# Performance work log

Measured on AMD Instinct MI355X. Metric: run time of the kernel, lower is better.

## Reference

```python
import jax, jax.numpy as jnp
import numpy as np

EMBED_DIM = 768
Q_DIM = 64
V_DIM = 64
WINDOW_SIZE = 3


def setup_inputs() -> dict:
    key = jax.random.key(0)
    ks = jax.random.split(key, 7)
    B, N = 4, 4096
    s = 1.0 / np.sqrt(EMBED_DIM)
    x = jax.random.normal(ks[0], (B, N, EMBED_DIM), dtype=jnp.float32)
    Wq = jax.random.normal(ks[1], (EMBED_DIM, Q_DIM), dtype=jnp.float32) * s
    bq = jax.random.normal(ks[2], (Q_DIM,), dtype=jnp.float32) * 0.01
    Wk = jax.random.normal(ks[3], (EMBED_DIM, Q_DIM), dtype=jnp.float32) * s
    bk = jax.random.normal(ks[4], (Q_DIM,), dtype=jnp.float32) * 0.01
    Wv = jax.random.normal(ks[5], (EMBED_DIM, V_DIM), dtype=jnp.float32) * s
    bv = jax.random.normal(ks[6], (V_DIM,), dtype=jnp.float32) * 0.01
    return {"x": x, "Wq": Wq, "bq": bq, "Wk": Wk, "bk": bk, "Wv": Wv, "bv": bv}


def reference(x, Wq, bq, Wk, bk, Wv, bv):
    # Faithful translation of SliddingWindowAttention.forward, including the
    # original's quirk: diagonal scores are written into columns 0..window_size-1
    # of a full (B, N, N) zero matrix, softmax is taken over ALL N columns
    # (zeros included), and the result is matmul'd with V.
    B, N, _ = x.shape
    Q = x @ Wq + bq  # (B, N, Q_DIM)
    K = x @ Wk + bk  # (B, N, Q_DIM)
    V = x @ Wv + bv  # (B, N, V_DIM)

    half = WINDOW_SIZE // 2
    columns = jnp.zeros((B, N, N), dtype=x.dtype)
    for idx, di in enumerate(range(-half, half + 1)):
        # diagonal offset di: pair row i with column j = i + di (valid rows only)
        rows = np.arange(max(0, -di), N - max(0, di))
        cols_j = rows + di
        c = jnp.einsum('bid,bid->bi', Q[:, rows, :], K[:, cols_j, :])
        columns = columns.at[:, rows, idx].set(c)

    attn = jax.nn.softmax(columns, axis=2)  # (B, N, N)
    return attn @ V  # (B, N, V_DIM)
```

## Files before the change

### kernel.cpp

```cpp
#include <hip/hip_runtime.h>
#include <math.h>

#define EMBED 768
#define NTOK  4096
#define NB    4
#define ROWS  16384
#define CN    192

typedef __attribute__((ext_vector_type(8))) short bf16x8;
typedef __attribute__((ext_vector_type(8))) unsigned short u16x8;
typedef __attribute__((ext_vector_type(4))) float f32x4;

__device__ inline void split2(float f, short& h, short& l) {
  union { float f; unsigned u; } a; a.f = f;
  unsigned r = (a.u + 0x7FFFu + ((a.u >> 16) & 1u)) & 0xFFFF0000u;
  h = (short)(r >> 16);
  union { unsigned u; float f; } hf; hf.u = r;
  union { float f; unsigned u; } b; b.f = f - hf.f;
  l = (short)((b.u + 0x7FFFu + ((b.u >> 16) & 1u)) >> 16);
}

__global__ __launch_bounds__(256) void wprep(const float* __restrict__ Wq,
                                             const float* __restrict__ Wk,
                                             const float* __restrict__ Wv,
                                             unsigned short* __restrict__ Wt,
                                             float* __restrict__ Vsum) {
  __shared__ float tile[32 * 64];
  const int b   = blockIdx.x;
  const int mat = b / 24;
  const int ks  = b - mat * 24;
  const float* W = (mat == 0) ? Wq : (mat == 1) ? Wk : Wv;
  const int t = threadIdx.x;

  const float4* src = (const float4*)(W + ks * 2048);
  ((float4*)tile)[t]       = src[t];
  ((float4*)tile)[t + 256] = src[t + 256];
  __syncthreads();

  const int n  = t >> 2;
  const int ko = (t & 3) * 8;
  u16x8 hv, lv;
#pragma unroll
  for (int j = 0; j < 8; ++j) {
    short h, l;
    split2(tile[(ko + j) * 64 + n], h, l);
    hv[j] = (unsigned short)h;
    lv[j] = (unsigned short)l;
  }
  const size_t base = (size_t)ks * 12288 + (size_t)(mat * 64 + n) * 32 + ko;
  *(u16x8*)(Wt + base)        = hv;
  *(u16x8*)(Wt + base + 6144) = lv;

  if (b == 0 && t < NB * 64) Vsum[t] = 0.f;
}

__device__ inline void cvt8(const float4 a0, const float4 a1, bf16x8& h, bf16x8& l) {
  const float f[8] = {a0.x, a0.y, a0.z, a0.w, a1.x, a1.y, a1.z, a1.w};
#pragma unroll
  for (int j = 0; j < 8; ++j) {
    union { float f; unsigned u; } a; a.f = f[j];
    unsigned th = a.u + 0x7FFFu + ((a.u >> 16) & 1u);
    h[j] = (short)(th >> 16);
    union { unsigned u; float f; } hf; hf.u = th & 0xFFFF0000u;
    union { float f; unsigned u; } r; r.f = f[j] - hf.f;
    unsigned tl = r.u + 0x7FFFu + ((r.u >> 16) & 1u);
    l[j] = (short)(tl >> 16);
  }
}

__device__ inline void loadA(const float* __restrict__ p, float4* d) {
  d[0] = *(const float4*)p;
  d[1] = *(const float4*)(p + 4);
}

__device__ inline void loadB(const unsigned short* __restrict__ p0,
                             const unsigned short* __restrict__ p1, bf16x8* d) {
#pragma unroll
  for (int nt = 0; nt < 6; ++nt) {
    d[nt]     = *(const bf16x8*)(p0 + (nt - 2) * 512);
    d[6 + nt] = *(const bf16x8*)(p1 + (nt - 2) * 512);
  }
}

__device__ inline void compute6(const float4* A, const bf16x8* B, f32x4* acc) {
  bf16x8 ah, al;
  cvt8(A[0], A[1], ah, al);
#pragma unroll
  for (int nt = 0; nt < 6; ++nt) {
    acc[nt] = __builtin_amdgcn_mfma_f32_16x16x32_bf16(ah, B[nt],     acc[nt], 0, 0, 0);
    acc[nt] = __builtin_amdgcn_mfma_f32_16x16x32_bf16(ah, B[6 + nt], acc[nt], 0, 0, 0);
    acc[nt] = __builtin_amdgcn_mfma_f32_16x16x32_bf16(al, B[nt],     acc[nt], 0, 0, 0);
  }
}

__global__ __launch_bounds__(256, 2) void qkv_mfma(const float* __restrict__ x,
                                                   const unsigned short* __restrict__ Wtu,
                                                   const float* __restrict__ bq,
                                                   const float* __restrict__ bk,
                                                   const float* __restrict__ bv,
                                                   float* __restrict__ C,
                                                   float* __restrict__ Vsum) {
  const int lane  = threadIdx.x & 63;
  const int wm    = (threadIdx.x >> 6) & 1;
  const int wn    = threadIdx.x >> 7;
  const int ml    = lane & 15;
  const int q     = lane >> 4;
  const int r0    = blockIdx.x * 32;
  const int nbase = wn * 96;

  f32x4 acc[6] = {};

  const float* xap = x + (size_t)(r0 + wm * 16 + ml) * EMBED + q * 8;
  const unsigned short* b0 = Wtu + (nbase + 32 + ml) * 32 + q * 8;
  const unsigned short* b1 = b0 + 6144;

  float4 A0[2], A1[2];
  bf16x8 B0[12], B1[12];

  loadA(xap, A0);
  loadB(b0, b1, B0);
  b0 += 12288; b1 += 12288;

  for (int ks = 0; ks < 24; ks += 2) {
    loadA(xap + 32, A1);
    loadB(b0, b1, B1);
    b0 += 12288; b1 += 12288;
    compute6(A0, B0, acc);
    if (ks < 22) {
      loadA(xap + 64, A0);
      loadB(b0, b1, B0);
      b0 += 12288; b1 += 12288;
    }
    xap += 64;
    compute6(A1, B1, acc);
  }

#pragma unroll
  for (int nt = 0; nt < 6; ++nt) {
    const int n = nbase + nt * 16 + ml;
    const float bias = (n < 64) ? bq[n] : (n < 128) ? bk[n - 64] : bv[n - 128];
#pragma unroll
    for (int reg = 0; reg < 4; ++reg) {
      const int row = r0 + wm * 16 + q * 4 + reg;
      C[(size_t)row * CN + n] = acc[nt][reg] + bias;
    }
  }

  if (wn == 1) {
#pragma unroll
    for (int nt = 2; nt < 6; ++nt) {
      const int n = nbase + nt * 16 + ml;
      float s = acc[nt][0] + acc[nt][1] + acc[nt][2] + acc[nt][3] + 4.f * bv[n - 128];
      s += __shfl_xor(s, 16, 64);
      s += __shfl_xor(s, 32, 64);
      if (q == 0) atomicAdd(&Vsum[(r0 >> 12) * 64 + (n - 128)], s);
    }
  }
}

__global__ __launch_bounds__(256) void attn_kernel(const float* __restrict__ C,
                                                   const float* __restrict__ Vsum,
                                                   float* __restrict__ out) {
  const int t    = threadIdx.x;
  const int lane = t & 63;
  const int wave = t >> 6;
  const int r = blockIdx.x * 4 + wave;
  const int b = r >> 12;
  const int i = r & (NTOK - 1);

  const float q  = C[(size_t)r * CN + lane];
  const float kc = C[(size_t)r * CN + 64 + lane];
  float km = 0.f, kp = 0.f;
  if (i > 0)        km = C[(size_t)(r - 1) * CN + 64 + lane];
  if (i < NTOK - 1) kp = C[(size_t)(r + 1) * CN + 64 + lane];

  float p0 = q * km, p1 = q * kc, p2 = q * kp;
#pragma unroll
  for (int off = 32; off > 0; off >>= 1) {
    p0 += __shfl_xor(p0, off, 64);
    p1 += __shfl_xor(p1, off, 64);
    p2 += __shfl_xor(p2, off, 64);
  }

  const float s0 = (i > 0) ? p0 : 0.f;
  const float s1 = p1;
  const float s2 = (i < NTOK - 1) ? p2 : 0.f;
  const float m  = fmaxf(fmaxf(s0, s1), fmaxf(s2, 0.f));
  const float e0 = expf(s0 - m);
  const float e1 = expf(s1 - m);
  const float e2 = expf(s2 - m);
  const float ez = expf(-m);
  const float Z  = e0 + e1 + e2 + (float)(NTOK - 3) * ez;

  const size_t vb = ((size_t)b * NTOK) * CN + 128;
  const float v0 = C[vb + lane];
  const float v1 = C[vb + CN + lane];
  const float v2 = C[vb + 2 * (size_t)CN + lane];
  const float vs = Vsum[b * 64 + lane];

  out[(size_t)r * 64 + lane] =
      (e0 * v0 + e1 * v1 + e2 * v2 + ez * (vs - v0 - v1 - v2)) / Z;
}

extern "C" void kernel_launch(void* const* d_in, const int* in_sizes, int n_in,
                              void* d_out, int out_size, void* d_ws, size_t ws_size,
                              hipStream_t stream) {
  const float* x  = (const float*)d_in[0];
  const float* Wq = (const float*)d_in[1];
  const float* bq = (const float*)d_in[2];
  const float* Wk = (const float*)d_in[3];
  const float* bk = (const float*)d_in[4];
  const float* Wv = (const float*)d_in[5];
  const float* bv = (const float*)d_in[6];
  float* out = (float*)d_out;

  float* C    = (float*)d_ws;
  float* Vsum = C + (size_t)ROWS * CN;
  unsigned short* Wt = (unsigned short*)(Vsum + NB * 64);

  wprep<<<72, 256, 0, stream>>>(Wq, Wk, Wv, Wt, Vsum);
  qkv_mfma<<<512, 256, 0, stream>>>(x, Wt, bq, bk, bv, C, Vsum);
  attn_kernel<<<ROWS / 4, 256, 0, stream>>>(C, Vsum, out);
}
```

Measured before the change: 143.9 us.

## Stage weight tiles into LDS via async global_load_lds double buffering

The QKV projection kernel now copies each 32-wide K-slice of the pre-split bf16 weights into a double-buffered shared-memory tile with the direct global-to-LDS load builtin. The per-wave B fragments are then read from LDS instead of being loaded separately from global memory by every wave, which cuts redundant global traffic and register pressure. It also simplifies the low-part rounding of the activation split. The cost is two block barriers per iteration and 48KB of LDS per block, which may limit occupancy.

```diff
diff --git a/kernel.cpp b/kernel.cpp
--- a/kernel.cpp
+++ b/kernel.cpp
@@ -18,6 +18,15 @@
   union { unsigned u; float f; } hf; hf.u = r;
   union { float f; unsigned u; } b; b.f = f - hf.f;
   l = (short)((b.u + 0x7FFFu + ((b.u >> 16) & 1u)) >> 16);
+}
+
+__device__ inline void splitA(float f, short& h, short& l) {
+  union { float f; unsigned u; } a; a.f = f;
+  unsigned r = (a.u + 0x7FFFu + ((a.u >> 16) & 1u)) & 0xFFFF0000u;
+  h = (short)(r >> 16);
+  union { unsigned u; float f; } hf; hf.u = r;
+  union { float f; unsigned u; } b; b.f = f - hf.f;
+  l = (short)((b.u + 0x8000u) >> 16);
 }
 
 __global__ __launch_bounds__(256) void wprep(const float* __restrict__ Wq,
@@ -54,44 +63,46 @@
   if (b == 0 && t < NB * 64) Vsum[t] = 0.f;
 }
 
-__device__ inline void cvt8(const float4 a0, const float4 a1, bf16x8& h, bf16x8& l) {
-  const float f[8] = {a0.x, a0.y, a0.z, a0.w, a1.x, a1.y, a1.z, a1.w};
-#pragma unroll
-  for (int j = 0; j < 8; ++j) {
-    union { float f; unsigned u; } a; a.f = f[j];
-    unsigned th = a.u + 0x7FFFu + ((a.u >> 16) & 1u);
-    h[j] = (short)(th >> 16);
-    union { unsigned u; float f; } hf; hf.u = th & 0xFFFF0000u;
-    union { float f; unsigned u; } r; r.f = f[j] - hf.f;
-    unsigned tl = r.u + 0x7FFFu + ((r.u >> 16) & 1u);
-    l[j] = (short)(tl >> 16);
-  }
-}
-
-__device__ inline void loadA(const float* __restrict__ p, float4* d) {
-  d[0] = *(const float4*)p;
-  d[1] = *(const float4*)(p + 4);
-}
-
-__device__ inline void loadB(const unsigned short* __restrict__ p0,
-                             const unsigned short* __restrict__ p1, bf16x8* d) {
-#pragma unroll
-  for (int nt = 0; nt < 6; ++nt) {
-    d[nt]     = *(const bf16x8*)(p0 + (nt - 2) * 512);
-    d[6 + nt] = *(const bf16x8*)(p1 + (nt - 2) * 512);
-  }
-}
-
-__device__ inline void compute6(const float4* A, const bf16x8* B, f32x4* acc) {
-  bf16x8 ah, al;
-  cvt8(A[0], A[1], ah, al);
-#pragma unroll
-  for (int nt = 0; nt < 6; ++nt) {
-    acc[nt] = __builtin_amdgcn_mfma_f32_16x16x32_bf16(ah, B[nt],     acc[nt], 0, 0, 0);
-    acc[nt] = __builtin_amdgcn_mfma_f32_16x16x32_bf16(ah, B[6 + nt], acc[nt], 0, 0, 0);
-    acc[nt] = __builtin_amdgcn_mfma_f32_16x16x32_bf16(al, B[nt],     acc[nt], 0, 0, 0);
-  }
-}
+__device__ inline void gload_lds16(const unsigned short* g, unsigned short* l) {
+  __builtin_amdgcn_global_load_lds(
+      (const __attribute__((address_space(1))) unsigned int*)(g),
+      (__attribute__((address_space(3))) unsigned int*)(l),
+      16, 0, 0);
+}
+
+#define STAGE(LB, KS) do {                                            \
+    const unsigned short* _g = Wtu + (size_t)(KS) * 12288 + tid * 8;  \
+    unsigned short* _l = (LB) + tid * 8;                              \
+    gload_lds16(_g,          _l);                                     \
+    gload_lds16(_g + 2048,   _l + 2048);                              \
+    gload_lds16(_g + 4096,   _l + 4096);                              \
+    gload_lds16(_g + 6144,   _l + 6144);                              \
+    gload_lds16(_g + 8192,   _l + 8192);                              \
+    gload_lds16(_g + 10240,  _l + 10240);                             \
+  } while (0)
+
+#define DO_NT(LBP, NT, ACC) do {                                               \
+    bf16x8 _bh = *(const bf16x8*)((LBP) + (NT) * 512);                         \
+    bf16x8 _bl = *(const bf16x8*)((LBP) + (NT) * 512 + 6144);                  \
+    ACC = __builtin_amdgcn_mfma_f32_16x16x32_bf16(ah, _bh, ACC, 0, 0, 0);      \
+    ACC = __builtin_amdgcn_mfma_f32_16x16x32_bf16(ah, _bl, ACC, 0, 0, 0);      \
+    ACC = __builtin_amdgcn_mfma_f32_16x16x32_bf16(al, _bh, ACC, 0, 0, 0);      \
+  } while (0)
+
+#define COMPUTE(LB, F0, F1) do {                                      \
+    bf16x8 ah, al; short _h, _l;                                      \
+    splitA((F0).x, _h, _l); ah[0] = _h; al[0] = _l;                   \
+    splitA((F0).y, _h, _l); ah[1] = _h; al[1] = _l;                   \
+    splitA((F0).z, _h, _l); ah[2] = _h; al[2] = _l;                   \
+    splitA((F0).w, _h, _l); ah[3] = _h; al[3] = _l;                   \
+    splitA((F1).x, _h, _l); ah[4] = _h; al[4] = _l;                   \
+    splitA((F1).y, _h, _l); ah[5] = _h; al[5] = _l;                   \
+    splitA((F1).z, _h, _l); ah[6] = _h; al[6] = _l;                   \
+    splitA((F1).w, _h, _l); ah[7] = _h; al[7] = _l;                   \
+    const unsigned short* _lb = (LB) + lboff;                         \
+    DO_NT(_lb, 0, acc0); DO_NT(_lb, 1, acc1); DO_NT(_lb, 2, acc2);    \
+    DO_NT(_lb, 3, acc3); DO_NT(_lb, 4, acc4); DO_NT(_lb, 5, acc5);    \
+  } while (0)
 
 __global__ __launch_bounds__(256, 2) void qkv_mfma(const float* __restrict__ x,
                                                    const unsigned short* __restrict__ Wtu,
@@ -100,61 +111,70 @@
                                                    const float* __restrict__ bv,
                                                    float* __restrict__ C,
                                                    float* __restrict__ Vsum) {
-  const int lane  = threadIdx.x & 63;
-  const int wm    = (threadIdx.x >> 6) & 1;
-  const int wn    = threadIdx.x >> 7;
+  __shared__ unsigned short lbuf0[12288];
+  __shared__ unsigned short lbuf1[12288];
+
+  const int tid   = threadIdx.x;
+  const int lane  = tid & 63;
+  const int wm    = (tid >> 6) & 1;
+  const int wn    = tid >> 7;
   const int ml    = lane & 15;
   const int q     = lane >> 4;
   const int r0    = blockIdx.x * 32;
   const int nbase = wn * 96;
-
-  f32x4 acc[6] = {};
+  const int lboff = (wn * 96 + ml) * 32 + q * 8;
+
+  f32x4 acc0 = {0.f, 0.f, 0.f, 0.f}, acc1 = {0.f, 0.f, 0.f, 0.f},
+        acc2 = {0.f, 0.f, 0.f, 0.f}, acc3 = {0.f, 0.f, 0.f, 0.f},
+        acc4 = {0.f, 0.f, 0.f, 0.f}, acc5 = {0.f, 0.f, 0.f, 0.f};
 
   const float* xap = x + (size_t)(r0 + wm * 16 + ml) * EMBED + q * 8;
-  const unsigned short* b0 = Wtu + (nbase + 32 + ml) * 32 + q * 8;
-  const unsigned short* b1 = b0 + 6144;
-
-  float4 A0[2], A1[2];
-  bf16x8 B0[12], B1[12];
-
-  loadA(xap, A0);
-  loadB(b0, b1, B0);
-  b0 += 12288; b1 += 12288;
+
+  STAGE(lbuf0, 0);
+  float4 a0 = *(const float4*)xap;
+  float4 a1 = *(const float4*)(xap + 4);
 
   for (int ks = 0; ks < 24; ks += 2) {
-    loadA(xap + 32, A1);
-    loadB(b0, b1, B1);
-    b0 += 12288; b1 += 12288;
-    compute6(A0, B0, acc);
+    __syncthreads();
+    STAGE(lbuf1, ks + 1);
+    float4 n0 = *(const float4*)(xap + 32);
+    float4 n1 = *(const float4*)(xap + 36);
+    COMPUTE(lbuf0, a0, a1);
+
+    __syncthreads();
     if (ks < 22) {
-      loadA(xap + 64, A0);
-      loadB(b0, b1, B0);
-      b0 += 12288; b1 += 12288;
+      STAGE(lbuf0, ks + 2);
+      float4 m0 = *(const float4*)(xap + 64);
+      float4 m1 = *(const float4*)(xap + 68);
+      a0 = m0; a1 = m1;
     }
+    COMPUTE(lbuf1, n0, n1);
     xap += 64;
-    compute6(A1, B1, acc);
-  }
-
-#pragma unroll
-  for (int nt = 0; nt < 6; ++nt) {
-    const int n = nbase + nt * 16 + ml;
-    const float bias = (n < 64) ? bq[n] : (n < 128) ? bk[n - 64] : bv[n - 128];
-#pragma unroll
-    for (int reg = 0; reg < 4; ++reg) {
-      const int row = r0 + wm * 16 + q * 4 + reg;
-      C[(size_t)row * CN + n] = acc[nt][reg] + bias;
-    }
-  }
+  }
+
+#define EPI(NT, ACC) do {                                                   \
+    const int n = nbase + (NT) * 16 + ml;                                   \
+    const float bias = (n < 64) ? bq[n] : (n < 128) ? bk[n - 64] : bv[n - 128]; \
+    const int row = r0 + wm * 16 + q * 4;                                   \
+    C[(size_t)(row + 0) * CN + n] = ACC[0] + bias;                          \
+    C[(size_t)(row + 1) * CN + n] = ACC[1] + bias;                          \
+    C[(size_t)(row + 2) * CN + n] = ACC[2] + bias;                          \
+    C[(size_t)(row + 3) * CN + n] = ACC[3] + bias;                          \
+  } while (0)
+
+  EPI(0, acc0); EPI(1, acc1); EPI(2, acc2);
+  EPI(3, acc3); EPI(4, acc4); EPI(5, acc5);
+
+#define VS(NT, ACC) do {                                                    \
+    const int n = nbase + (NT) * 16 + ml;                                   \
+    float s = ACC[0] + ACC[1] + ACC[2] + ACC[3] + 4.f * bv[n - 128];        \
+    s += __shfl_xor(s, 16, 64);                                             \
+    s += __shfl_xor(s, 32, 64);                                             \
+    if (q == 0) atomicAdd(&Vsum[(r0 >> 12) * 64 + (n - 128)], s);           \
+  } while (0)
 
   if (wn == 1) {
-#pragma unroll
-    for (int nt = 2; nt < 6; ++nt) {
-      const int n = nbase + nt * 16 + ml;
-      float s = acc[nt][0] + acc[nt][1] + acc[nt][2] + acc[nt][3] + 4.f * bv[n - 128];
-      s += __shfl_xor(s, 16, 64);
-      s += __shfl_xor(s, 32, 64);
-      if (q == 0) atomicAdd(&Vsum[(r0 >> 12) * 64 + (n - 128)], s);
-    }
+    VS(2, acc2); VS(3, acc3); VS(4, acc4); VS(5, acc5);
   }
 }
 
```

After: 128.2 us. 10.9% less time.
